# Performance work log

Measured on AMD Instinct MI355X. Metric: run time of the kernel, lower is better.

The kernel has to match this reference:

```python
import jax, jax.numpy as jnp
import numpy as np

NUM_CLASSES = 200
NUM_FEATURES = 128
NUM_PROTO_PER_CLASS = 10
NUM_PROTOTYPES = NUM_CLASSES * NUM_PROTO_PER_CLASS
EPS = 1e-4
INCORRECT_STRENGTH = -0.5


def _make_last_layer_weight():
    # prototype_class_identity[j, j // num_proto_per_class] = 1; weight = correct + (-0.5)*incorrect
    proto_ids = np.arange(NUM_PROTOTYPES) // NUM_PROTO_PER_CLASS  # (P,)
    correct = (np.arange(NUM_CLASSES)[:, None] == proto_ids[None, :]).astype(np.float32)  # (C, P)
    weight = correct + INCORRECT_STRENGTH * (1.0 - correct)
    return jnp.asarray(weight)


def setup_inputs() -> dict:
    key = jax.random.key(0)
    k1, k2 = jax.random.split(key)
    features = jax.random.normal(k1, (64, NUM_FEATURES, 14, 14), dtype=jnp.float32)
    # SHIFTED_NORMAL prototype init: small-variance normal shifted by 0.5
    prototypes = 0.5 + 0.1 * jax.random.normal(k2, (NUM_PROTOTYPES, NUM_FEATURES, 1, 1), dtype=jnp.float32)
    last_weight = _make_last_layer_weight()  # (C, P)
    return {"features": features, "prototypes": prototypes, "last_weight": last_weight}


def reference(features, prototypes, last_weight):
    # features: (N, D, H, W); prototypes: (P, D, 1, 1); last_weight: (C, P)
    protos = prototypes[:, :, 0, 0]  # (P, D)
    x_sq = jnp.sum(features * features, axis=1, keepdims=True)  # (N, 1, H, W)
    p_sq = jnp.sum(protos * protos, axis=1)  # (P,)
    xp = jnp.einsum("ndhw,pd->nphw", features, protos)  # (N, P, H, W)
    dist = jax.nn.relu(x_sq + p_sq[None, :, None, None] - 2.0 * xp)  # (N, P, H, W)
    sim = jnp.log((dist + 1.0) / (dist + EPS))  # (N, P, H, W)
    sim_max = jnp.max(sim.reshape(sim.shape[0], sim.shape[1], -1), axis=2)  # (N, P)
    logits = sim_max @ last_weight.T  # (N, C)
    min_dist = jnp.min(dist.reshape(dist.shape[0], dist.shape[1], -1), axis=2)  # (N, P)
    return (logits, min_dist)
```

## Files before the change

kernel.cpp:

```cpp
#include <hip/hip_runtime.h>
#include <hip/hip_bf16.h>

#define NUM_CLASSES 200
#define NF 128
#define NP 2000
#define NPC 10
#define HW 196
#define MPAD 208
#define NB 64
#define EPSV 1e-4f
#define TROW 17
#define PTILE 250
#define CTILE 25

typedef __attribute__((ext_vector_type(8))) short short8;
typedef __attribute__((ext_vector_type(4))) float f32x4;

static __device__ __forceinline__ unsigned short f2bf(float x) {
    __hip_bfloat16 h = __float2bfloat16(x);
    return __builtin_bit_cast(unsigned short, h);
}

static __device__ __forceinline__ void gl_lds16(const void* g, void* l) {
    __builtin_amdgcn_global_load_lds(
        (const __attribute__((address_space(1))) void*)g,
        (__attribute__((address_space(3))) void*)l, 16, 0, 0);
}
static __device__ __forceinline__ void gl_lds4(const void* g, void* l) {
    __builtin_amdgcn_global_load_lds(
        (const __attribute__((address_space(1))) void*)g,
        (__attribute__((address_space(3))) void*)l, 4, 0, 0);
}

__global__ __launch_bounds__(256) void kprep(const float* __restrict__ f,
                                             const float* __restrict__ protos,
                                             uint4* __restrict__ G,
                                             float* __restrict__ xsqG,
                                             unsigned short* __restrict__ pB,
                                             float* __restrict__ psqG,
                                             float* __restrict__ logits) {
    __shared__ float tile[NF * TROW];

    const int n  = blockIdx.x;
    const int mt = blockIdx.y;
    const int t  = threadIdx.x;

    if (mt == 13) {
        const int rl  = t >> 3;
        const int sub = t & 7;
        const int p   = n * 32 + rl;
        if (p < NP) {
            const float* pr = protos + (size_t)p * NF + sub * 16;
            float xp = 0.f;
            unsigned short u[16];
            #pragma unroll
            for (int q = 0; q < 4; ++q) {
                float4 v = *(const float4*)(pr + q * 4);
                xp += v.x * v.x + v.y * v.y + v.z * v.z + v.w * v.w;
                u[q * 4 + 0] = f2bf(v.x); u[q * 4 + 1] = f2bf(v.y);
                u[q * 4 + 2] = f2bf(v.z); u[q * 4 + 3] = f2bf(v.w);
            }
            uint4* dst = (uint4*)(pB + (size_t)p * NF + sub * 16);
            dst[0] = ((uint4*)u)[0];
            dst[1] = ((uint4*)u)[1];
            xp += __shfl_xor(xp, 1, 64);
            xp += __shfl_xor(xp, 2, 64);
            xp += __shfl_xor(xp, 4, 64);
            if (sub == 0) psqG[p] = xp;
        }
        return;
    }

    if (mt == 0 && t < NUM_CLASSES) logits[(size_t)n * NUM_CLASSES + t] = 0.f;

    const int hw0 = mt * 16;
    const int kb  = t >> 2;
    const int hwl = (t & 3) * 4;
    float4 v0 = make_float4(0.f, 0.f, 0.f, 0.f), v1 = v0;
    if (hw0 + hwl + 4 <= HW) {
        v0 = *(const float4*)(f + ((size_t)n * NF + kb) * HW + hw0 + hwl);
        v1 = *(const float4*)(f + ((size_t)n * NF + kb + 64) * HW + hw0 + hwl);
    }
    tile[kb * TROW + hwl + 0] = v0.x;
    tile[kb * TROW + hwl + 1] = v0.y;
    tile[kb * TROW + hwl + 2] = v0.z;
    tile[kb * TROW + hwl + 3] = v0.w;
    tile[(kb + 64) * TROW + hwl + 0] = v1.x;
    tile[(kb + 64) * TROW + hwl + 1] = v1.y;
    tile[(kb + 64) * TROW + hwl + 2] = v1.z;
    tile[(kb + 64) * TROW + hwl + 3] = v1.w;
    __syncthreads();

    const int hwl2 = t >> 4;
    const int kg   = t & 15;
    float xp = 0.f;
    unsigned short u[8];
    #pragma unroll
    for (int j = 0; j < 8; ++j) {
        float val = tile[(kg * 8 + j) * TROW + hwl2];
        xp += val * val;
        u[j] = f2bf(val);
    }
    G[((size_t)n * MPAD + hw0 + hwl2) * 16 + (kg ^ hwl2)] = *(uint4*)u;

    xp += __shfl_xor(xp, 1, 64);
    xp += __shfl_xor(xp, 2, 64);
    xp += __shfl_xor(xp, 4, 64);
    xp += __shfl_xor(xp, 8, 64);
    if (kg == 0) xsqG[(size_t)n * 256 + hw0 + hwl2] = (hw0 + hwl2 < HW) ? xp : 3.0e38f;
}

__global__ __launch_bounds__(256, 2) void kdist(const uint4* __restrict__ G,
                                                const float* __restrict__ xsqG,
                                                const unsigned short* __restrict__ pB,
                                                const float* __restrict__ psqG,
                                                const float* __restrict__ W,
                                                float* __restrict__ min_out,
                                                float* __restrict__ logits) {
    __shared__ unsigned short sf[MPAD * NF];
    __shared__ float sxsq[256];
    __shared__ float scsum[32];
    float* const ssim = (float*)sf;

    const int n    = blockIdx.x;
    const int pt   = blockIdx.y;
    const int t    = threadIdx.x;
    const int wave = t >> 6;
    const int lane = t & 63;
    const int row  = lane & 15;
    const int quad = lane >> 4;
    const int sb   = wave * 64;
    const int p0   = pt * PTILE;

    gl_lds4(xsqG + (size_t)n * 256 + t, (char*)sxsq + (size_t)wave * 64 * 4);
    const uint4* gsrc = G + (size_t)n * (MPAD * 16);
    #pragma unroll
    for (int i = 0; i < 13; ++i)
        gl_lds16(gsrc + i * 256 + t, (char*)sf + ((size_t)i * 256 + wave * 64) * 16);

    short8 A[4][4];
    #pragma unroll
    for (int g = 0; g < 4; ++g) {
        int p = p0 + sb + g * 16 + row;
        const short8* pr = (const short8*)(pB + (size_t)(p < NP ? p : NP - 1) * NF);
        #pragma unroll
        for (int kk = 0; kk < 4; ++kk)
            A[g][kk] = pr[quad + kk * 4];
    }

    __syncthreads();

    float runmin[4][4];
    #pragma unroll
    for (int g = 0; g < 4; ++g)
        #pragma unroll
        for (int r = 0; r < 4; ++r) runmin[g][r] = 3.0e38f;

    const short8* sfv = (const short8*)sf;
    for (int mt = 0; mt < 13; ++mt) {
        const int base = (mt * 16 + row) * 16;
        short8 b0 = sfv[base + ((quad + 0)  ^ row)];
        short8 b1 = sfv[base + ((quad + 4)  ^ row)];
        short8 b2 = sfv[base + ((quad + 8)  ^ row)];
        short8 b3 = sfv[base + ((quad + 12) ^ row)];
        float xv = sxsq[mt * 16 + row];

        #pragma unroll
        for (int g = 0; g < 4; ++g) {
            f32x4 acc = {0.f, 0.f, 0.f, 0.f};
            acc = __builtin_amdgcn_mfma_f32_16x16x32_bf16(A[g][0], b0, acc, 0, 0, 0);
            acc = __builtin_amdgcn_mfma_f32_16x16x32_bf16(A[g][1], b1, acc, 0, 0, 0);
            acc = __builtin_amdgcn_mfma_f32_16x16x32_bf16(A[g][2], b2, acc, 0, 0, 0);
            acc = __builtin_amdgcn_mfma_f32_16x16x32_bf16(A[g][3], b3, acc, 0, 0, 0);
            #pragma unroll
            for (int r = 0; r < 4; ++r)
                runmin[g][r] = fminf(runmin[g][r], xv - 2.f * acc[r]);
        }
    }

    __syncthreads();

    #pragma unroll
    for (int g = 0; g < 4; ++g) {
        #pragma unroll
        for (int off = 1; off < 16; off <<= 1)
            #pragma unroll
            for (int r = 0; r < 4; ++r)
                runmin[g][r] = fminf(runmin[g][r], __shfl_xor(runmin[g][r], off, 64));
        #pragma unroll
        for (int r = 0; r < 4; ++r) {
            int slot = sb + g * 16 + quad * 4 + r;
            if (row == 0) {
                float sim = 0.f;
                if (slot < PTILE) {
                    float m = fmaxf(runmin[g][r] + psqG[p0 + slot], 0.f);
                    min_out[(size_t)n * NP + p0 + slot] = m;
                    sim = logf((m + 1.f) / (m + EPSV));
                }
                ssim[slot] = sim;
            }
        }
    }
    __syncthreads();

    if (t < CTILE) {
        float s = 0.f;
        #pragma unroll
        for (int j = 0; j < NPC; ++j) s += ssim[t * NPC + j];
        scsum[t] = s;
    }
    __syncthreads();

    if (t < NUM_CLASSES) {
        const float a = W[0];
        const float b = W[NPC];
        float tp = 0.f;
        #pragma unroll
        for (int j = 0; j < CTILE; ++j) tp += scsum[j];
        float v = b * tp;
        const int c0 = pt * CTILE;
        if (t >= c0 && t < c0 + CTILE) v += (a - b) * scsum[t - c0];
        atomicAdd(&logits[(size_t)n * NUM_CLASSES + t], v);
    }
}

extern "C" void kernel_launch(void* const* d_in, const int* in_sizes, int n_in,
                              void* d_out, int out_size, void* d_ws, size_t ws_size,
                              hipStream_t stream) {
    const float* f      = (const float*)d_in[0];
    const float* protos = (const float*)d_in[1];
    const float* W      = (const float*)d_in[2];

    float* logits   = (float*)d_out;
    float* min_dist = (float*)d_out + NB * NUM_CLASSES;

    unsigned short* pB = (unsigned short*)d_ws;
    float* psqG = (float*)((char*)d_ws + 512000);
    uint4* G    = (uint4*)((char*)d_ws + 524288);
    float* xsqG = (float*)((char*)d_ws + 524288 + (size_t)NB * MPAD * 16 * sizeof(uint4));

    kprep<<<dim3(NB, 14), 256, 0, stream>>>(f, protos, G, xsqG, pB, psqG, logits);
    kdist<<<dim3(NB, 8), 256, 0, stream>>>(G, xsqG, pB, psqG, W, min_dist, logits);
}
```

Baseline: 77.08 us.

## Load feature fragments directly from global memory instead of staging in LDS

The prep kernel now writes the bf16 feature tile in an MFMA-fragment-ordered layout, so each lane of the distance kernel can read its B operands straight from global/L2 memory with coalesced loads. The ~53KB LDS staging buffer, the global-to-LDS copies and their barrier are removed, and the occupancy hint rises from 2 to 3 blocks per CU. The cost is that every wave re-reads the same feature fragments from cache inside a non-unrolled loop, which exposes global load latency per iteration instead of LDS latency.

```diff
diff --git a/kernel.cpp b/kernel.cpp
--- a/kernel.cpp
+++ b/kernel.cpp
@@ -6,7 +6,7 @@
 #define NP 2000
 #define NPC 10
 #define HW 196
-#define MPAD 208
+#define NCH 13
 #define NB 64
 #define EPSV 1e-4f
 #define TROW 17
@@ -21,20 +21,9 @@
     return __builtin_bit_cast(unsigned short, h);
 }
 
-static __device__ __forceinline__ void gl_lds16(const void* g, void* l) {
-    __builtin_amdgcn_global_load_lds(
-        (const __attribute__((address_space(1))) void*)g,
-        (__attribute__((address_space(3))) void*)l, 16, 0, 0);
-}
-static __device__ __forceinline__ void gl_lds4(const void* g, void* l) {
-    __builtin_amdgcn_global_load_lds(
-        (const __attribute__((address_space(1))) void*)g,
-        (__attribute__((address_space(3))) void*)l, 4, 0, 0);
-}
-
 __global__ __launch_bounds__(256) void kprep(const float* __restrict__ f,
                                              const float* __restrict__ protos,
-                                             uint4* __restrict__ G,
+                                             uint4* __restrict__ G2,
                                              float* __restrict__ xsqG,
                                              unsigned short* __restrict__ pB,
                                              float* __restrict__ psqG,
@@ -101,7 +90,8 @@
         xp += val * val;
         u[j] = f2bf(val);
     }
-    G[((size_t)n * MPAD + hw0 + hwl2) * 16 + (kg ^ hwl2)] = *(uint4*)u;
+    G2[((size_t)(n * NCH + mt)) * 256 + (kg >> 2) * 64 + (kg & 3) * 16 + hwl2]
+        = *(uint4*)u;
 
     xp += __shfl_xor(xp, 1, 64);
     xp += __shfl_xor(xp, 2, 64);
@@ -110,17 +100,15 @@
     if (kg == 0) xsqG[(size_t)n * 256 + hw0 + hwl2] = (hw0 + hwl2 < HW) ? xp : 3.0e38f;
 }
 
-__global__ __launch_bounds__(256, 2) void kdist(const uint4* __restrict__ G,
+__global__ __launch_bounds__(256, 3) void kdist(const short8* __restrict__ G2,
                                                 const float* __restrict__ xsqG,
                                                 const unsigned short* __restrict__ pB,
                                                 const float* __restrict__ psqG,
                                                 const float* __restrict__ W,
                                                 float* __restrict__ min_out,
                                                 float* __restrict__ logits) {
-    __shared__ unsigned short sf[MPAD * NF];
-    __shared__ float sxsq[256];
+    __shared__ float ssim[256];
     __shared__ float scsum[32];
-    float* const ssim = (float*)sf;
 
     const int n    = blockIdx.x;
     const int pt   = blockIdx.y;
@@ -132,12 +120,6 @@
     const int sb   = wave * 64;
     const int p0   = pt * PTILE;
 
-    gl_lds4(xsqG + (size_t)n * 256 + t, (char*)sxsq + (size_t)wave * 64 * 4);
-    const uint4* gsrc = G + (size_t)n * (MPAD * 16);
-    #pragma unroll
-    for (int i = 0; i < 13; ++i)
-        gl_lds16(gsrc + i * 256 + t, (char*)sf + ((size_t)i * 256 + wave * 64) * 16);
-
     short8 A[4][4];
     #pragma unroll
     for (int g = 0; g < 4; ++g) {
@@ -148,22 +130,22 @@
             A[g][kk] = pr[quad + kk * 4];
     }
 
-    __syncthreads();
-
     float runmin[4][4];
     #pragma unroll
     for (int g = 0; g < 4; ++g)
         #pragma unroll
         for (int r = 0; r < 4; ++r) runmin[g][r] = 3.0e38f;
 
-    const short8* sfv = (const short8*)sf;
-    for (int mt = 0; mt < 13; ++mt) {
-        const int base = (mt * 16 + row) * 16;
-        short8 b0 = sfv[base + ((quad + 0)  ^ row)];
-        short8 b1 = sfv[base + ((quad + 4)  ^ row)];
-        short8 b2 = sfv[base + ((quad + 8)  ^ row)];
-        short8 b3 = sfv[base + ((quad + 12) ^ row)];
-        float xv = sxsq[mt * 16 + row];
+    const short8* gb  = G2 + (size_t)n * (NCH * 256) + quad * 16 + row;
+    const float*  xsb = xsqG + (size_t)n * 256 + row;
+
+    #pragma unroll 1
+    for (int mt = 0; mt < NCH; ++mt) {
+        short8 b0 = gb[mt * 256 +   0];
+        short8 b1 = gb[mt * 256 +  64];
+        short8 b2 = gb[mt * 256 + 128];
+        short8 b3 = gb[mt * 256 + 192];
+        float  xv = xsb[mt * 16];
 
         #pragma unroll
         for (int g = 0; g < 4; ++g) {
@@ -177,8 +159,6 @@
                 runmin[g][r] = fminf(runmin[g][r], xv - 2.f * acc[r]);
         }
     }
-
-    __syncthreads();
 
     #pragma unroll
     for (int g = 0; g < 4; ++g) {
@@ -236,9 +216,10 @@
 
     unsigned short* pB = (unsigned short*)d_ws;
     float* psqG = (float*)((char*)d_ws + 512000);
-    uint4* G    = (uint4*)((char*)d_ws + 524288);
-    float* xsqG = (float*)((char*)d_ws + 524288 + (size_t)NB * MPAD * 16 * sizeof(uint4));
-
-    kprep<<<dim3(NB, 14), 256, 0, stream>>>(f, protos, G, xsqG, pB, psqG, logits);
-    kdist<<<dim3(NB, 8), 256, 0, stream>>>(G, xsqG, pB, psqG, W, min_dist, logits);
-}
+    uint4* G2   = (uint4*)((char*)d_ws + 524288);
+    float* xsqG = (float*)((char*)d_ws + 524288 + (size_t)NB * NCH * 256 * sizeof(uint4));
+
+    kprep<<<dim3(NB, 14), 256, 0, stream>>>(f, protos, G2, xsqG, pB, psqG, logits);
+    kdist<<<dim3(NB, 8), 256, 0, stream>>>((const short8*)G2, xsqG, pB, psqG, W,
+                                           min_dist, logits);
+}
```

New measurement: 79.43 us. +3.0%, slower.
